# Kernel optimization log

Measured on AMD Instinct MI355X. Metric: run time of the kernel, lower is better.

The kernel has to match this reference:

```python
import jax, jax.numpy as jnp
import numpy as np

N, E, D = 50000, 800000, 128  # nodes, edges, node_dim == edge_dim
EPS = 1e-5

def _mlp(x, w1, b1, w2, b2, w3, b3):
    h = jax.nn.silu(x @ w1 + b1)
    h = jax.nn.silu(h @ w2 + b2)
    return h @ w3 + b3

def _ln(x, g, b):
    m = jnp.mean(x, axis=-1, keepdims=True)
    v = jnp.var(x, axis=-1, keepdims=True)
    return (x - m) * jax.lax.rsqrt(v + EPS) * g + b

def setup_inputs() -> dict:
    key = jax.random.key(0)
    ks = jax.random.split(key, 20)
    s = 0.02
    inp = {
        "x": jax.random.normal(ks[0], (N, D), jnp.float32),
        "edge_index": jax.random.randint(ks[1], (2, E), 0, N, jnp.int64 if jax.config.jax_enable_x64 else jnp.int32),
        "edge_attr": jax.random.normal(ks[2], (E, D), jnp.float32),
        # edge MLP: [2D+D, D, D, D]
        "ew1": jax.random.normal(ks[3], (3 * D, D), jnp.float32) * s,
        "eb1": jnp.zeros((D,), jnp.float32),
        "ew2": jax.random.normal(ks[4], (D, D), jnp.float32) * s,
        "eb2": jnp.zeros((D,), jnp.float32),
        "ew3": jax.random.normal(ks[5], (D, D), jnp.float32) * s,
        "eb3": jnp.zeros((D,), jnp.float32),
        "eln_g": jnp.ones((D,), jnp.float32),
        "eln_b": jnp.zeros((D,), jnp.float32),
        # node MLP: [D+D, D, D, D]
        "nw1": jax.random.normal(ks[6], (2 * D, D), jnp.float32) * s,
        "nb1": jnp.zeros((D,), jnp.float32),
        "nw2": jax.random.normal(ks[7], (D, D), jnp.float32) * s,
        "nb2": jnp.zeros((D,), jnp.float32),
        "nw3": jax.random.normal(ks[8], (D, D), jnp.float32) * s,
        "nb3": jnp.zeros((D,), jnp.float32),
        "nln_g": jnp.ones((D,), jnp.float32),
        "nln_b": jnp.zeros((D,), jnp.float32),
    }
    return inp

def reference(x, edge_index, edge_attr,
              ew1, eb1, ew2, eb2, ew3, eb3, eln_g, eln_b,
              nw1, nb1, nw2, nb2, nw3, nb3, nln_g, nln_b):
    i, j = edge_index[0], edge_index[1]
    # Edge processor: gather endpoints, concat, MLP+LN, residual
    e_in = jnp.concatenate([x[i], x[j], edge_attr], axis=-1)  # [E, 3D]
    e_out = _ln(_mlp(e_in, ew1, eb1, ew2, eb2, ew3, eb3), eln_g, eln_b)
    edge_attr_new = edge_attr + e_out  # [E, D]
    # Node processor: scatter-add by j, concat, MLP+LN, residual
    agg = jax.ops.segment_sum(edge_attr_new, j, num_segments=x.shape[0])  # [N, D]
    n_in = jnp.concatenate([x, agg], axis=-1)  # [N, 2D]
    n_out = _ln(_mlp(n_in, nw1, nb1, nw2, nb2, nw3, nb3), nln_g, nln_b)
    x_new = x + n_out
    return (x_new, edge_attr_new)
```

## Files before the change

kernel.cpp:

```cpp
#include <hip/hip_runtime.h>
#include <hip/hip_bf16.h>
#include <math.h>

#define NNODE 50000
#define NEDGE 800000
#define DD 128

typedef __bf16 bf16x8 __attribute__((ext_vector_type(8)));
typedef __bf16 bf16x4 __attribute__((ext_vector_type(4)));
typedef float f32x4 __attribute__((ext_vector_type(4)));

#define MFMA_BF16 __builtin_amdgcn_mfma_f32_16x16x32_bf16

#define WPK_TOTAL 147456

__global__ void pack_weights(const float* ew1, const float* ew2, const float* ew3,
                             const float* nw1, const float* nw2, const float* nw3,
                             __bf16* out) {
    int t = blockIdx.x * 256 + threadIdx.x;
    if (t >= WPK_TOTAL) return;
    const float* W; int base;
    if (t < 49152)       { W = ew1; base = 0; }
    else if (t < 65536)  { W = ew2; base = 49152; }
    else if (t < 81920)  { W = ew3; base = 65536; }
    else if (t < 114688) { W = nw1; base = 81920; }
    else if (t < 131072) { W = nw2; base = 114688; }
    else                 { W = nw3; base = 131072; }
    int local = t - base;
    int frag = local >> 9;
    int rem  = local & 511;
    int lane = rem >> 3;
    int j    = rem & 7;
    int kc = frag >> 3, nt = frag & 7;
    int k = kc * 32 + (lane >> 4) * 8 + j;
    int n = nt * 16 + (lane & 15);
    out[t] = (__bf16)W[k * 128 + n];
}

__global__ void count_edges(const int* __restrict__ ei, int* __restrict__ cursor) {
    int e = blockIdx.x * 256 + threadIdx.x;
    if (e < NEDGE) atomicAdd(&cursor[ei[NEDGE + e]], 1);
}

__global__ void scan_offsets(int* __restrict__ cursor ,
                             int* __restrict__ offsets) {
    __shared__ int lsum[1024];
    const int t = threadIdx.x;
    const int CH = (NNODE + 1023) / 1024;
    const int base = t * CH;
    int s = 0;
    for (int i = 0; i < CH; ++i) {
        int idx = base + i;
        if (idx < NNODE) s += cursor[idx];
    }
    lsum[t] = s;
    __syncthreads();
    for (int off = 1; off < 1024; off <<= 1) {
        int v = lsum[t];
        int u = (t >= off) ? lsum[t - off] : 0;
        __syncthreads();
        lsum[t] = v + u;
        __syncthreads();
    }
    int prefix = (t == 0) ? 0 : lsum[t - 1];
    for (int i = 0; i < CH; ++i) {
        int idx = base + i;
        if (idx < NNODE) {
            int c = cursor[idx];
            offsets[idx] = prefix;
            cursor[idx] = prefix;
            prefix += c;
        }
    }
    if (t == 1023) offsets[NNODE] = prefix;
}

__global__ void fill_elist(const int* __restrict__ ei, int* __restrict__ cursor,
                           int* __restrict__ elist) {
    int e = blockIdx.x * 256 + threadIdx.x;
    if (e < NEDGE) {
        int pos = atomicAdd(&cursor[ei[NEDGE + e]], 1);
        elist[pos] = e;
    }
}

template <int KC, int STRIDE>
__device__ inline void mm_stage(const __bf16* ldsA, int colbase,
                                const __bf16* wpk, int woff,
                                int l, int l15, int quad, int w,
                                f32x4 acc[4][2]) {
    for (int kc = 0; kc < KC; ++kc) {
        bf16x8 a[4];
#pragma unroll
        for (int rt = 0; rt < 4; ++rt)
            a[rt] = *(const bf16x8*)&ldsA[(rt * 16 + l15) * STRIDE + colbase + kc * 32 + quad * 8];
        bf16x8 b[2];
#pragma unroll
        for (int nh = 0; nh < 2; ++nh) {
            int nt = 2 * w + nh;
            b[nh] = *(const bf16x8*)&wpk[woff + (kc * 8 + nt) * 512 + l * 8];
        }
#pragma unroll
        for (int rt = 0; rt < 4; ++rt)
#pragma unroll
            for (int nh = 0; nh < 2; ++nh)
                acc[rt][nh] = MFMA_BF16(a[rt], b[nh], acc[rt][nh], 0, 0, 0);
    }
}

template <int STRIDE>
__device__ inline void silu_store(const f32x4 acc[4][2], float bc0, float bc1,
                                  __bf16* ldsH, int colbase,
                                  int l15, int quad, int w) {
#pragma unroll
    for (int rt = 0; rt < 4; ++rt)
#pragma unroll
        for (int nh = 0; nh < 2; ++nh) {
            int col = (2 * w + nh) * 16 + l15;
            float bc = nh ? bc1 : bc0;
#pragma unroll
            for (int reg = 0; reg < 4; ++reg) {
                float v = acc[rt][nh][reg] + bc;
                v = v / (1.0f + __expf(-v));
                int row = rt * 16 + quad * 4 + reg;
                ldsH[row * STRIDE + colbase + col] = (__bf16)v;
            }
        }
}

__global__ __launch_bounds__(256, 3) void edge_kernel(
    const float* __restrict__ x, const int* __restrict__ ei, const float* __restrict__ ea,
    const __bf16* __restrict__ wpk,
    const float* __restrict__ eb1, const float* __restrict__ eb2, const float* __restrict__ eb3,
    const float* __restrict__ lng, const float* __restrict__ lnb,
    float* __restrict__ out) {
    __shared__ __bf16 lds_e[64 * 392];
    __shared__ float lds_part[64][8];
    __shared__ int lds_i[64], lds_j[64];

    const int tid = threadIdx.x;
    const int l = tid & 63, w = tid >> 6;
    const int l15 = l & 15, quad = l >> 4;
    const int e0 = blockIdx.x * 64;

    const int col0 = (2 * w) * 16 + l15, col1 = col0 + 16;
    const float b1c0 = eb1[col0], b1c1 = eb1[col1];
    const float b2c0 = eb2[col0], b2c1 = eb2[col1];
    const float b3c0 = eb3[col0], b3c1 = eb3[col1];
    const float g0 = lng[col0], g1 = lng[col1];
    const float lb0 = lnb[col0], lb1 = lnb[col1];

    if (tid < 64) lds_i[tid] = ei[e0 + tid];
    else if (tid < 128) lds_j[tid - 64] = ei[NEDGE + e0 + (tid - 64)];
    __syncthreads();

    for (int t = tid; t < 64 * 96; t += 256) {
        int row = t / 96;
        int q = t - row * 96;
        int seg = q >> 5, c = q & 31;
        const float* src;
        if (seg == 0)      src = x + (size_t)lds_i[row] * 128 + c * 4;
        else if (seg == 1) src = x + (size_t)lds_j[row] * 128 + c * 4;
        else               src = ea + (size_t)(e0 + row) * 128 + c * 4;
        float4 v = *(const float4*)src;
        bf16x4 bv = { (__bf16)v.x, (__bf16)v.y, (__bf16)v.z, (__bf16)v.w };
        *(bf16x4*)&lds_e[row * 392 + seg * 128 + c * 4] = bv;
    }
    __syncthreads();

    f32x4 acc[4][2] = {};
    mm_stage<12, 392>(lds_e, 0, wpk, 0, l, l15, quad, w, acc);
    __syncthreads();
    silu_store<392>(acc, b1c0, b1c1, lds_e, 0, l15, quad, w);
    __syncthreads();

    f32x4 acc2[4][2] = {};
    mm_stage<4, 392>(lds_e, 0, wpk, 49152, l, l15, quad, w, acc2);
    silu_store<392>(acc2, b2c0, b2c1, lds_e, 128, l15, quad, w);
    __syncthreads();

    f32x4 acc3[4][2] = {};
    mm_stage<4, 392>(lds_e, 128, wpk, 65536, l, l15, quad, w, acc3);

#pragma unroll
    for (int rt = 0; rt < 4; ++rt)
#pragma unroll
        for (int reg = 0; reg < 4; ++reg) {
            float v0 = acc3[rt][0][reg] + b3c0;
            float v1 = acc3[rt][1][reg] + b3c1;
            float s = v0 + v1, q = v0 * v0 + v1 * v1;
#pragma unroll
            for (int off = 1; off < 16; off <<= 1) {
                s += __shfl_xor(s, off);
                q += __shfl_xor(q, off);
            }
            if (l15 == 0) {
                int row = rt * 16 + quad * 4 + reg;
                lds_part[row][2 * w] = s;
                lds_part[row][2 * w + 1] = q;
            }
        }
    __syncthreads();

#pragma unroll
    for (int rt = 0; rt < 4; ++rt)
#pragma unroll
        for (int reg = 0; reg < 4; ++reg) {
            int row = rt * 16 + quad * 4 + reg;
            float4 p0 = *(const float4*)&lds_part[row][0];
            float4 p1 = *(const float4*)&lds_part[row][4];
            float stot = p0.x + p0.z + p1.x + p1.z;
            float qtot = p0.y + p0.w + p1.y + p1.w;
            float mean = stot * (1.0f / 128.0f);
            float var = qtot * (1.0f / 128.0f) - mean * mean;
            float rstd = rsqrtf(var + 1e-5f);
            int e = e0 + row;
#pragma unroll
            for (int nh = 0; nh < 2; ++nh) {
                int col = (2 * w + nh) * 16 + l15;
                float v = acc3[rt][nh][reg] + (nh ? b3c1 : b3c0);
                float o = (v - mean) * rstd * (nh ? g1 : g0) + (nh ? lb1 : lb0);
                float res = o + (float)lds_e[row * 392 + 256 + col];
                out[(size_t)NNODE * 128 + (size_t)e * 128 + col] = res;
            }
        }
}

__global__ __launch_bounds__(256, 3) void node_kernel(
    const float* __restrict__ x, const __bf16* __restrict__ wpk,
    const int* __restrict__ offsets, const int* __restrict__ elist,
    const float* __restrict__ nb1, const float* __restrict__ nb2, const float* __restrict__ nb3,
    const float* __restrict__ lng, const float* __restrict__ lnb,
    float* __restrict__ out) {
    __shared__ __bf16 lds_n[64 * 264];
    __shared__ float lds_part[64][8];

    const int tid = threadIdx.x;
    const int l = tid & 63, w = tid >> 6;
    const int l15 = l & 15, quad = l >> 4;
    const int r0 = blockIdx.x * 64;

    const int col0 = (2 * w) * 16 + l15, col1 = col0 + 16;
    const float b1c0 = nb1[col0], b1c1 = nb1[col1];
    const float b2c0 = nb2[col0], b2c1 = nb2[col1];
    const float b3c0 = nb3[col0], b3c1 = nb3[col1];
    const float g0 = lng[col0], g1 = lng[col1];
    const float lb0 = lnb[col0], lb1 = lnb[col1];

    const float* eout = out + (size_t)NNODE * 128;

    for (int t = tid; t < 64 * 32; t += 256) {
        int row = t >> 5, c = t & 31;
        int r = r0 + row;
        f32x4 v = {0.f, 0.f, 0.f, 0.f};
        if (r < NNODE) v = *(const f32x4*)(x + (size_t)r * 128 + c * 4);
        bf16x4 bv = { (__bf16)v[0], (__bf16)v[1], (__bf16)v[2], (__bf16)v[3] };
        *(bf16x4*)&lds_n[row * 264 + c * 4] = bv;
    }

    {
        const int g = tid & 15;
        for (int round = 0; round < 4; ++round) {
            int row = round * 16 + (tid >> 4);
            int r = r0 + row;
            f32x4 a0 = {0.f, 0.f, 0.f, 0.f}, a1 = a0, a2 = a0, a3 = a0;
            if (r < NNODE) {
                int k = offsets[r], kend = offsets[r + 1];
                for (; k + 2 <= kend; k += 2) {
                    int ec0 = elist[k], ec1 = elist[k + 1];
                    const f32x4* p0 = (const f32x4*)(eout + (size_t)ec0 * 128);
                    const f32x4* p1 = (const f32x4*)(eout + (size_t)ec1 * 128);
                    f32x4 v00 = p0[g], v01 = p0[g + 16];
                    f32x4 v10 = p1[g], v11 = p1[g + 16];
                    a0 += v00; a1 += v01; a2 += v10; a3 += v11;
                }
                if (k < kend) {
                    const f32x4* p0 = (const f32x4*)(eout + (size_t)elist[k] * 128);
                    a0 += p0[g]; a1 += p0[g + 16];
                }
            }
            a0 += a2; a1 += a3;
            bf16x4 b0 = { (__bf16)a0[0], (__bf16)a0[1], (__bf16)a0[2], (__bf16)a0[3] };
            bf16x4 b1 = { (__bf16)a1[0], (__bf16)a1[1], (__bf16)a1[2], (__bf16)a1[3] };
            *(bf16x4*)&lds_n[row * 264 + 128 + g * 4] = b0;
            *(bf16x4*)&lds_n[row * 264 + 128 + 64 + g * 4] = b1;
        }
    }
    __syncthreads();

    f32x4 acc[4][2] = {};
    mm_stage<8, 264>(lds_n, 0, wpk, 81920, l, l15, quad, w, acc);
    __syncthreads();
    silu_store<264>(acc, b1c0, b1c1, lds_n, 0, l15, quad, w);
    __syncthreads();

    f32x4 acc2[4][2] = {};
    mm_stage<4, 264>(lds_n, 0, wpk, 114688, l, l15, quad, w, acc2);
    silu_store<264>(acc2, b2c0, b2c1, lds_n, 128, l15, quad, w);
    __syncthreads();

    f32x4 acc3[4][2] = {};
    mm_stage<4, 264>(lds_n, 128, wpk, 131072, l, l15, quad, w, acc3);

#pragma unroll
    for (int rt = 0; rt < 4; ++rt)
#pragma unroll
        for (int reg = 0; reg < 4; ++reg) {
            float v0 = acc3[rt][0][reg] + b3c0;
            float v1 = acc3[rt][1][reg] + b3c1;
            float s = v0 + v1, q = v0 * v0 + v1 * v1;
#pragma unroll
            for (int off = 1; off < 16; off <<= 1) {
                s += __shfl_xor(s, off);
                q += __shfl_xor(q, off);
            }
            if (l15 == 0) {
                int row = rt * 16 + quad * 4 + reg;
                lds_part[row][2 * w] = s;
                lds_part[row][2 * w + 1] = q;
            }
        }
    __syncthreads();

#pragma unroll
    for (int rt = 0; rt < 4; ++rt)
#pragma unroll
        for (int reg = 0; reg < 4; ++reg) {
            int row = rt * 16 + quad * 4 + reg;
            int r = r0 + row;
            if (r >= NNODE) continue;
            float4 p0 = *(const float4*)&lds_part[row][0];
            float4 p1 = *(const float4*)&lds_part[row][4];
            float stot = p0.x + p0.z + p1.x + p1.z;
            float qtot = p0.y + p0.w + p1.y + p1.w;
            float mean = stot * (1.0f / 128.0f);
            float var = qtot * (1.0f / 128.0f) - mean * mean;
            float rstd = rsqrtf(var + 1e-5f);
#pragma unroll
            for (int nh = 0; nh < 2; ++nh) {
                int col = (2 * w + nh) * 16 + l15;
                float v = acc3[rt][nh][reg] + (nh ? b3c1 : b3c0);
                float o = (v - mean) * rstd * (nh ? g1 : g0) + (nh ? lb1 : lb0);
                float res = o + x[(size_t)r * 128 + col];
                out[(size_t)r * 128 + col] = res;
            }
        }
}

extern "C" void kernel_launch(void* const* d_in, const int* in_sizes, int n_in,
                              void* d_out, int out_size, void* d_ws, size_t ws_size,
                              hipStream_t stream) {
    const float* x    = (const float*)d_in[0];
    const int*   ei   = (const int*)  d_in[1];
    const float* ea   = (const float*)d_in[2];
    const float* ew1  = (const float*)d_in[3];
    const float* eb1  = (const float*)d_in[4];
    const float* ew2  = (const float*)d_in[5];
    const float* eb2  = (const float*)d_in[6];
    const float* ew3  = (const float*)d_in[7];
    const float* eb3  = (const float*)d_in[8];
    const float* elng = (const float*)d_in[9];
    const float* elnb = (const float*)d_in[10];
    const float* nw1  = (const float*)d_in[11];
    const float* nb1  = (const float*)d_in[12];
    const float* nw2  = (const float*)d_in[13];
    const float* nb2  = (const float*)d_in[14];
    const float* nw3  = (const float*)d_in[15];
    const float* nb3  = (const float*)d_in[16];
    const float* nlng = (const float*)d_in[17];
    const float* nlnb = (const float*)d_in[18];
    float* out = (float*)d_out;

    char* ws = (char*)d_ws;
    __bf16* wpk  = (__bf16*)ws;
    int* offsets = (int*)(ws + 294912);
    int* cursor  = (int*)(ws + 495616);
    int* elist   = (int*)(ws + 696320);

    hipMemsetAsync(cursor, 0, NNODE * sizeof(int), stream);
    pack_weights<<<(WPK_TOTAL + 255) / 256, 256, 0, stream>>>(ew1, ew2, ew3, nw1, nw2, nw3, wpk);
    count_edges<<<(NEDGE + 255) / 256, 256, 0, stream>>>(ei, cursor);
    scan_offsets<<<1, 1024, 0, stream>>>(cursor, offsets);
    fill_elist<<<(NEDGE + 255) / 256, 256, 0, stream>>>(ei, cursor, elist);
    edge_kernel<<<NEDGE / 64, 256, 0, stream>>>(x, ei, ea, wpk, eb1, eb2, eb3, elng, elnb, out);
    node_kernel<<<(NNODE + 63) / 64, 256, 0, stream>>>(x, wpk, offsets, elist,
                                                       nb1, nb2, nb3, nlng, nlnb, out);
}
```

Before: 1.450 ms.

## Split edge layer-1 GEMM into three K-chunks with double-buffered LDS and prefetch

The edge kernel no longer stages the full 64x384 concatenated input in LDS. It loads the x[i], x[j] and edge_attr chunks one at a time into two small 136-stride buffers, issuing each global load before the previous chunk's MFMA stage so memory latency overlaps compute. This shrinks LDS use and lets launch bounds rise to 4 blocks per SM for both kernels, which may increase register pressure or spilling. The node aggregation loop is also unrolled to four edges per iteration to put more loads in flight.

```diff
diff --git a/kernel.cpp b/kernel.cpp
--- a/kernel.cpp
+++ b/kernel.cpp
@@ -128,13 +128,15 @@
         }
 }
 
-__global__ __launch_bounds__(256, 3) void edge_kernel(
+#define ESTR 136
+__global__ __launch_bounds__(256, 4) void edge_kernel(
     const float* __restrict__ x, const int* __restrict__ ei, const float* __restrict__ ea,
     const __bf16* __restrict__ wpk,
     const float* __restrict__ eb1, const float* __restrict__ eb2, const float* __restrict__ eb3,
     const float* __restrict__ lng, const float* __restrict__ lnb,
     float* __restrict__ out) {
-    __shared__ __bf16 lds_e[64 * 392];
+    __shared__ __bf16 buf0[64 * ESTR];
+    __shared__ __bf16 buf1[64 * ESTR];
     __shared__ float lds_part[64][8];
     __shared__ int lds_i[64], lds_j[64];
 
@@ -154,33 +156,68 @@
     else if (tid < 128) lds_j[tid - 64] = ei[NEDGE + e0 + (tid - 64)];
     __syncthreads();
 
-    for (int t = tid; t < 64 * 96; t += 256) {
-        int row = t / 96;
-        int q = t - row * 96;
-        int seg = q >> 5, c = q & 31;
-        const float* src;
-        if (seg == 0)      src = x + (size_t)lds_i[row] * 128 + c * 4;
-        else if (seg == 1) src = x + (size_t)lds_j[row] * 128 + c * 4;
-        else               src = ea + (size_t)(e0 + row) * 128 + c * 4;
-        float4 v = *(const float4*)src;
-        bf16x4 bv = { (__bf16)v.x, (__bf16)v.y, (__bf16)v.z, (__bf16)v.w };
-        *(bf16x4*)&lds_e[row * 392 + seg * 128 + c * 4] = bv;
-    }
-    __syncthreads();
-
+    float4 xr[8];
+
+#pragma unroll
+    for (int c = 0; c < 8; ++c) {
+        int idx = tid + c * 256;
+        int row = idx >> 5, f4 = idx & 31;
+        xr[c] = *(const float4*)(x + (size_t)lds_i[row] * 128 + f4 * 4);
+    }
+#pragma unroll
+    for (int c = 0; c < 8; ++c) {
+        int idx = tid + c * 256;
+        int row = idx >> 5, f4 = idx & 31;
+        bf16x4 bv = { (__bf16)xr[c].x, (__bf16)xr[c].y, (__bf16)xr[c].z, (__bf16)xr[c].w };
+        *(bf16x4*)&buf0[row * ESTR + f4 * 4] = bv;
+    }
+    __syncthreads();
+
+#pragma unroll
+    for (int c = 0; c < 8; ++c) {
+        int idx = tid + c * 256;
+        int row = idx >> 5, f4 = idx & 31;
+        xr[c] = *(const float4*)(x + (size_t)lds_j[row] * 128 + f4 * 4);
+    }
     f32x4 acc[4][2] = {};
-    mm_stage<12, 392>(lds_e, 0, wpk, 0, l, l15, quad, w, acc);
-    __syncthreads();
-    silu_store<392>(acc, b1c0, b1c1, lds_e, 0, l15, quad, w);
+    mm_stage<4, ESTR>(buf0, 0, wpk, 0, l, l15, quad, w, acc);
+#pragma unroll
+    for (int c = 0; c < 8; ++c) {
+        int idx = tid + c * 256;
+        int row = idx >> 5, f4 = idx & 31;
+        bf16x4 bv = { (__bf16)xr[c].x, (__bf16)xr[c].y, (__bf16)xr[c].z, (__bf16)xr[c].w };
+        *(bf16x4*)&buf1[row * ESTR + f4 * 4] = bv;
+    }
+    __syncthreads();
+
+#pragma unroll
+    for (int c = 0; c < 8; ++c) {
+        int idx = tid + c * 256;
+        int row = idx >> 5, f4 = idx & 31;
+        xr[c] = *(const float4*)(ea + (size_t)(e0 + row) * 128 + f4 * 4);
+    }
+    mm_stage<4, ESTR>(buf1, 0, wpk, 16384, l, l15, quad, w, acc);
+#pragma unroll
+    for (int c = 0; c < 8; ++c) {
+        int idx = tid + c * 256;
+        int row = idx >> 5, f4 = idx & 31;
+        bf16x4 bv = { (__bf16)xr[c].x, (__bf16)xr[c].y, (__bf16)xr[c].z, (__bf16)xr[c].w };
+        *(bf16x4*)&buf0[row * ESTR + f4 * 4] = bv;
+    }
+    __syncthreads();
+
+    mm_stage<4, ESTR>(buf0, 0, wpk, 32768, l, l15, quad, w, acc);
+    silu_store<ESTR>(acc, b1c0, b1c1, buf1, 0, l15, quad, w);
     __syncthreads();
 
     f32x4 acc2[4][2] = {};
-    mm_stage<4, 392>(lds_e, 0, wpk, 49152, l, l15, quad, w, acc2);
-    silu_store<392>(acc2, b2c0, b2c1, lds_e, 128, l15, quad, w);
+    mm_stage<4, ESTR>(buf1, 0, wpk, 49152, l, l15, quad, w, acc2);
+    __syncthreads();
+    silu_store<ESTR>(acc2, b2c0, b2c1, buf1, 0, l15, quad, w);
     __syncthreads();
 
     f32x4 acc3[4][2] = {};
-    mm_stage<4, 392>(lds_e, 128, wpk, 65536, l, l15, quad, w, acc3);
+    mm_stage<4, ESTR>(buf1, 0, wpk, 65536, l, l15, quad, w, acc3);
 
 #pragma unroll
     for (int rt = 0; rt < 4; ++rt)
@@ -220,13 +257,13 @@
                 int col = (2 * w + nh) * 16 + l15;
                 float v = acc3[rt][nh][reg] + (nh ? b3c1 : b3c0);
                 float o = (v - mean) * rstd * (nh ? g1 : g0) + (nh ? lb1 : lb0);
-                float res = o + (float)lds_e[row * 392 + 256 + col];
+                float res = o + (float)buf0[row * ESTR + col];
                 out[(size_t)NNODE * 128 + (size_t)e * 128 + col] = res;
             }
         }
 }
 
-__global__ __launch_bounds__(256, 3) void node_kernel(
+__global__ __launch_bounds__(256, 4) void node_kernel(
     const float* __restrict__ x, const __bf16* __restrict__ wpk,
     const int* __restrict__ offsets, const int* __restrict__ elist,
     const float* __restrict__ nb1, const float* __restrict__ nb2, const float* __restrict__ nb3,
@@ -266,13 +303,26 @@
             f32x4 a0 = {0.f, 0.f, 0.f, 0.f}, a1 = a0, a2 = a0, a3 = a0;
             if (r < NNODE) {
                 int k = offsets[r], kend = offsets[r + 1];
+                for (; k + 4 <= kend; k += 4) {
+                    int ec0 = elist[k], ec1 = elist[k + 1];
+                    int ec2 = elist[k + 2], ec3 = elist[k + 3];
+                    const f32x4* p0 = (const f32x4*)(eout + (size_t)ec0 * 128);
+                    const f32x4* p1 = (const f32x4*)(eout + (size_t)ec1 * 128);
+                    const f32x4* p2 = (const f32x4*)(eout + (size_t)ec2 * 128);
+                    const f32x4* p3 = (const f32x4*)(eout + (size_t)ec3 * 128);
+                    f32x4 u0 = p0[g], u1 = p0[g + 16];
+                    f32x4 u2 = p1[g], u3 = p1[g + 16];
+                    f32x4 u4 = p2[g], u5 = p2[g + 16];
+                    f32x4 u6 = p3[g], u7 = p3[g + 16];
+                    a0 += u0; a1 += u1; a2 += u2; a3 += u3;
+                    a0 += u4; a1 += u5; a2 += u6; a3 += u7;
+                }
                 for (; k + 2 <= kend; k += 2) {
                     int ec0 = elist[k], ec1 = elist[k + 1];
                     const f32x4* p0 = (const f32x4*)(eout + (size_t)ec0 * 128);
                     const f32x4* p1 = (const f32x4*)(eout + (size_t)ec1 * 128);
-                    f32x4 v00 = p0[g], v01 = p0[g + 16];
-                    f32x4 v10 = p1[g], v11 = p1[g + 16];
-                    a0 += v00; a1 += v01; a2 += v10; a3 += v11;
+                    a0 += p0[g]; a1 += p0[g + 16];
+                    a2 += p1[g]; a3 += p1[g + 16];
                 }
                 if (k < kend) {
                     const f32x4* p0 = (const f32x4*)(eout + (size_t)elist[k] * 128);
```

After: 1.296 ms. 1.12x faster.
